# Kernel optimization log

Measured on AMD Instinct MI355X. Metric: run time of the kernel, lower is better.

Reference implementation:

```python
import jax, jax.numpy as jnp
import numpy as np

N_SRC = 50000
N_DST = 50000
E = 640000
D_IN = 128
D_OUT = 128
H = 4
D_HEAD = D_OUT // H


def setup_inputs() -> dict:
    key = jax.random.key(0)
    k1, k2, k3, k4, k5, k6 = jax.random.split(key, 6)
    src_feat = jax.random.normal(k1, (N_SRC, D_IN), dtype=jnp.float32)
    dst_feat = jax.random.normal(k2, (N_DST, D_IN), dtype=jnp.float32)
    src_idx = jax.random.randint(k3, (E,), 0, N_SRC)
    dst_idx = jax.random.randint(k4, (E,), 0, N_DST)
    edge_index = jnp.stack([src_idx, dst_idx], axis=0)  # [2, E]
    # nn.Linear(d_in, d_out, bias=False): store as [d_in, d_out] so h = x @ W
    W = jax.random.normal(k5, (D_IN, D_OUT), dtype=jnp.float32) * (1.0 / np.sqrt(D_IN))
    # nn.Linear(2*d_head, 1, bias=False): attention vector of length 2*d_head
    a = jax.random.normal(k6, (2 * D_HEAD,), dtype=jnp.float32) * (1.0 / np.sqrt(2 * D_HEAD))
    return {"src_feat": src_feat, "dst_feat": dst_feat, "edge_index": edge_index,
            "W": W, "a": a, "num_dst": N_DST}


def reference(src_feat, dst_feat, edge_index, W, a, num_dst):
    # Dropout in eval mode (identity).
    d_out = W.shape[1]
    d_head = d_out // H
    src_idx = edge_index[0]
    dst_idx = edge_index[1]

    h_src = (src_feat @ W).reshape(-1, H, d_head)  # [N_src, H, d_head]
    h_dst = (dst_feat @ W).reshape(-1, H, d_head)  # [N_dst, H, d_head]
    h_src_e = h_src[src_idx]                        # [E, H, d_head]
    h_dst_e = h_dst[dst_idx]                        # [E, H, d_head]

    # a^T [h_src || h_dst] == h_src . a_src + h_dst . a_dst (shared across heads)
    a_src, a_dst = a[:d_head], a[d_head:]
    e = jax.nn.elu(jnp.einsum('ehd,d->eh', h_src_e, a_src)
                   + jnp.einsum('ehd,d->eh', h_dst_e, a_dst))  # [E, H]

    # Segment softmax over edges grouped by destination node.
    e_max = jax.ops.segment_max(e, dst_idx, num_segments=num_dst)      # [N_dst, H]
    exp_e = jnp.exp(e - e_max[dst_idx])
    denom = jax.ops.segment_sum(exp_e, dst_idx, num_segments=num_dst)  # [N_dst, H]
    alpha = exp_e / (denom[dst_idx] + 1e-12)                           # [E, H]

    # Scatter-add of weighted messages.
    out = jax.ops.segment_sum(alpha[..., None] * h_src_e, dst_idx,
                              num_segments=num_dst)                    # [N_dst, H, d_head]
    return out.reshape(num_dst, d_out)
```

## Files before the change

### kernel.cpp

```cpp
#include <hip/hip_runtime.h>
#include <math.h>

constexpr int N_SRC_ = 50000;
constexpr int N_DST_ = 50000;
constexpr int N_TOT_ = 100000;
constexpr int E_     = 640000;
constexpr int D_     = 128;
constexpr int CAP_   = 64;
constexpr int NTILE  = (N_SRC_ + 31) / 32;
constexpr int MMB    = (NTILE + 3) / 4;

typedef float f32x4  __attribute__((ext_vector_type(4)));
typedef short bf16x8 __attribute__((ext_vector_type(8)));

union U4 { unsigned int u[4]; bf16x8 v; };

static __device__ __forceinline__ unsigned short f2bf_rne(float f) {
    unsigned int x = __float_as_uint(f);
    return (unsigned short)((x + 0x7FFFu + ((x >> 16) & 1u)) >> 16);
}

__global__ __launch_bounds__(256) void k_s2v(
    const float* __restrict__ src, const float* __restrict__ dst,
    const float* __restrict__ W, const float* __restrict__ a,
    float* __restrict__ s, int* __restrict__ cursor)
{
    __shared__ float val[128 * 8];
    const int t = threadIdx.x;

    int cid = blockIdx.x * 256 + t;
    if (cid < N_DST_) cursor[cid] = 0;

#pragma unroll
    for (int j = 0; j < 4; ++j) {
        int pair = t * 4 + j;
        int k = pair >> 3, col = pair & 7;
        int half = col >> 2, hd = col & 3;
        float acc = 0.f;
        for (int c2 = 0; c2 < 32; ++c2)
            acc += W[(size_t)k * 128 + hd * 32 + c2] * a[half * 32 + c2];
        val[k * 8 + col] = acc;
    }
    __syncthreads();

    const int gw = (blockIdx.x * 256 + t) >> 6;
    const int lane = t & 63;
    const int l32 = lane & 31, hf = lane >> 5;

    float4 vs[4], vd[4];
#pragma unroll
    for (int j = 0; j < 4; ++j) {
        vs[j] = *(const float4*)&val[(4 * l32 + j) * 8];
        vd[j] = *(const float4*)&val[(4 * l32 + j) * 8 + 4];
    }

    for (int p = gw; p < N_TOT_ / 2; p += 2048) {
        int node = p * 2 + hf;
        bool is_src = node < N_SRC_;
        const float* f = is_src ? src + (size_t)node * D_
                                : dst + (size_t)(node - N_SRC_) * D_;
        float4 x = *(const float4*)(f + l32 * 4);
        float4 v0 = is_src ? vs[0] : vd[0];
        float4 v1 = is_src ? vs[1] : vd[1];
        float4 v2 = is_src ? vs[2] : vd[2];
        float4 v3 = is_src ? vs[3] : vd[3];
        float a0 = x.x * v0.x + x.y * v1.x + x.z * v2.x + x.w * v3.x;
        float a1 = x.x * v0.y + x.y * v1.y + x.z * v2.y + x.w * v3.y;
        float a2 = x.x * v0.z + x.y * v1.z + x.z * v2.z + x.w * v3.z;
        float a3 = x.x * v0.w + x.y * v1.w + x.z * v2.w + x.w * v3.w;
#pragma unroll
        for (int m = 1; m < 32; m <<= 1) {
            a0 += __shfl_xor(a0, m, 64);
            a1 += __shfl_xor(a1, m, 64);
            a2 += __shfl_xor(a2, m, 64);
            a3 += __shfl_xor(a3, m, 64);
        }
        if (l32 == 0)
            *(float4*)&s[(size_t)node * 4] = make_float4(a0, a1, a2, a3);
    }
}

__global__ __launch_bounds__(256) void k_mm(
    const float* __restrict__ src, const float* __restrict__ W,
    unsigned int* __restrict__ h)
{
    __shared__ unsigned short wl[128 * 128];
    const int t = threadIdx.x;
    {
        const int n = t >> 1, half = t & 1;
#pragma unroll
        for (int c8 = 0; c8 < 8; ++c8) {
            int c = half * 8 + c8;
            U4 P;
#pragma unroll
            for (int q = 0; q < 4; ++q) {
                float f0 = W[(size_t)(c * 8 + 2 * q) * 128 + n];
                float f1 = W[(size_t)(c * 8 + 2 * q + 1) * 128 + n];
                P.u[q] = (unsigned int)f2bf_rne(f0)
                       | ((unsigned int)f2bf_rne(f1) << 16);
            }
            int slot = c ^ (n & 15);
            *(bf16x8*)&wl[n * 128 + slot * 8] = P.v;
        }
    }
    __syncthreads();

    const int wid = t >> 6, lane = t & 63;
    const int g = lane >> 4, sidx = lane & 15;
    const int wtile = blockIdx.x * 4 + wid;
    if (wtile >= NTILE) return;
    const int base = wtile * 32;
    const int r0 = base + sidx;
    const int r1g = base + 16 + sidx;
    const int r1 = (r1g < N_SRC_) ? r1g : 0;
    const float* p0 = src + (size_t)r0 * D_;
    const float* p1 = src + (size_t)r1 * D_;

    f32x4 acc[2][8];
#pragma unroll
    for (int m = 0; m < 2; ++m)
#pragma unroll
        for (int nf = 0; nf < 8; ++nf) acc[m][nf] = (f32x4)0.f;

#pragma unroll
    for (int ks = 0; ks < 4; ++ks) {
        const int k0 = ks * 32 + g * 8;
        bf16x8 af[2];
#pragma unroll
        for (int m = 0; m < 2; ++m) {
            const float* p = m ? p1 : p0;
            float4 v0 = *(const float4*)(p + k0);
            float4 v1 = *(const float4*)(p + k0 + 4);
            float f[8] = {v0.x, v0.y, v0.z, v0.w, v1.x, v1.y, v1.z, v1.w};
            U4 P;
#pragma unroll
            for (int q = 0; q < 4; ++q)
                P.u[q] = (unsigned int)f2bf_rne(f[2 * q])
                       | ((unsigned int)f2bf_rne(f[2 * q + 1]) << 16);
            af[m] = P.v;
        }
#pragma unroll
        for (int nf = 0; nf < 8; ++nf) {
            const int n = nf * 16 + sidx;
            const int off = n * 128 + ((ks * 4 + g) ^ sidx) * 8;
            bf16x8 b = *(const bf16x8*)&wl[off];
            acc[0][nf] = __builtin_amdgcn_mfma_f32_16x16x32_bf16(af[0], b, acc[0][nf], 0, 0, 0);
            acc[1][nf] = __builtin_amdgcn_mfma_f32_16x16x32_bf16(af[1], b, acc[1][nf], 0, 0, 0);
        }
    }

#pragma unroll
    for (int m = 0; m < 2; ++m) {
        const int rowb = base + m * 16 + g * 4;
#pragma unroll
        for (int r = 0; r < 4; ++r) {
            const int row = rowb + r;
            if (row < N_SRC_) {
#pragma unroll
                for (int q = 0; q < 4; ++q) {
                    unsigned int val = (unsigned int)f2bf_rne(acc[m][2 * q][r])
                                     | ((unsigned int)f2bf_rne(acc[m][2 * q + 1][r]) << 16);
                    h[(size_t)row * 64 + q * 16 + sidx] = val;
                }
            }
        }
    }
}

__global__ __launch_bounds__(256) void k_scatter(
    const int* __restrict__ src_idx, const int* __restrict__ dst_idx,
    const float* __restrict__ s,
    int* __restrict__ cursor, uint4* __restrict__ bucket)
{
    int e = blockIdx.x * 256 + threadIdx.x;
    int sn = src_idx[e], dn = dst_idx[e];
    float4 vsv = *(const float4*)&s[(size_t)sn * 4];
    float4 vdv = *(const float4*)&s[(size_t)(N_SRC_ + dn) * 4];
    float x0 = vsv.x + vdv.x, x1 = vsv.y + vdv.y;
    float x2 = vsv.z + vdv.z, x3 = vsv.w + vdv.w;
    float w0 = __expf(x0 > 0.f ? x0 : (__expf(x0) - 1.f));
    float w1 = __expf(x1 > 0.f ? x1 : (__expf(x1) - 1.f));
    float w2 = __expf(x2 > 0.f ? x2 : (__expf(x2) - 1.f));
    float w3 = __expf(x3 > 0.f ? x3 : (__expf(x3) - 1.f));
    uint4 ent;
    ent.x = (unsigned int)sn;
    ent.y = (unsigned int)f2bf_rne(w0) | ((unsigned int)f2bf_rne(w1) << 16);
    ent.z = (unsigned int)f2bf_rne(w2) | ((unsigned int)f2bf_rne(w3) << 16);
    ent.w = 0u;
    int pos = atomicAdd(&cursor[dn], 1);
    if (pos < CAP_) bucket[(size_t)dn * CAP_ + pos] = ent;
}

__global__ __launch_bounds__(256) void k_gather(
    const unsigned int* __restrict__ h2, const int* __restrict__ cursor,
    const uint4* __restrict__ bucket, float* __restrict__ out)
{
    int wid = (blockIdx.x * 256 + threadIdx.x) >> 6;
    int lane = threadIdx.x & 63;
    if (wid >= N_DST_) return;
    int cnt = min(cursor[wid], CAP_);
    const int hd = lane >> 4;
    const int sub = lane & 15;
    const uint4* B = bucket + (size_t)wid * CAP_;

    auto wext = [&](const uint4& e) {
        unsigned int u = (hd & 2) ? e.z : e.y;
        return __uint_as_float((hd & 1) ? (u & 0xFFFF0000u) : (u << 16));
    };

    float2 A[4] = {make_float2(0.f, 0.f), make_float2(0.f, 0.f),
                   make_float2(0.f, 0.f), make_float2(0.f, 0.f)};
    float dacc[4] = {0.f, 0.f, 0.f, 0.f};

    int i = 0;
    for (; i + 8 <= cnt; i += 8) {
        uint4 e[8];
        unsigned int v[8];
#pragma unroll
        for (int j = 0; j < 8; ++j) e[j] = B[i + j];
#pragma unroll
        for (int j = 0; j < 8; ++j) v[j] = h2[(size_t)e[j].x * 64 + lane];
#pragma unroll
        for (int j = 0; j < 8; ++j) {
            float w = wext(e[j]);
            dacc[j & 3] += w;
            A[j & 3].x = fmaf(w, __uint_as_float(v[j] << 16), A[j & 3].x);
            A[j & 3].y = fmaf(w, __uint_as_float(v[j] & 0xFFFF0000u), A[j & 3].y);
        }
    }
    for (; i + 4 <= cnt; i += 4) {
        uint4 e[4];
        unsigned int v[4];
#pragma unroll
        for (int j = 0; j < 4; ++j) e[j] = B[i + j];
#pragma unroll
        for (int j = 0; j < 4; ++j) v[j] = h2[(size_t)e[j].x * 64 + lane];
#pragma unroll
        for (int j = 0; j < 4; ++j) {
            float w = wext(e[j]);
            dacc[j] += w;
            A[j].x = fmaf(w, __uint_as_float(v[j] << 16), A[j].x);
            A[j].y = fmaf(w, __uint_as_float(v[j] & 0xFFFF0000u), A[j].y);
        }
    }
    for (; i < cnt; ++i) {
        uint4 e = B[i];
        unsigned int v = h2[(size_t)e.x * 64 + lane];
        float w = wext(e);
        dacc[0] += w;
        A[0].x = fmaf(w, __uint_as_float(v << 16), A[0].x);
        A[0].y = fmaf(w, __uint_as_float(v & 0xFFFF0000u), A[0].y);
    }

    float den = (dacc[0] + dacc[1]) + (dacc[2] + dacc[3]);
    float2 acc = make_float2((A[0].x + A[1].x) + (A[2].x + A[3].x),
                             (A[0].y + A[1].y) + (A[2].y + A[3].y));
    float inv = 1.f / (den + 1e-12f);
    out[(size_t)wid * D_ + 32 * hd + sub]      = acc.x * inv;
    out[(size_t)wid * D_ + 32 * hd + sub + 16] = acc.y * inv;
}

extern "C" void kernel_launch(void* const* d_in, const int* in_sizes, int n_in,
                              void* d_out, int out_size, void* d_ws, size_t ws_size,
                              hipStream_t stream)
{
    const float* src_feat = (const float*)d_in[0];
    const float* dst_feat = (const float*)d_in[1];
    const int*   edge     = (const int*)d_in[2];
    const int*   src_idx  = edge;
    const int*   dst_idx  = edge + E_;
    const float* W        = (const float*)d_in[3];
    const float* a        = (const float*)d_in[4];
    float*       out      = (float*)d_out;

    char* p = (char*)d_ws;
    auto alloc = [&](size_t bytes) {
        char* r = p;
        p += (bytes + 255) & ~(size_t)255;
        return r;
    };
    unsigned int* h = (unsigned int*)alloc((size_t)N_SRC_ * 64 * 4);
    float* s        = (float*)alloc((size_t)N_TOT_ * 4 * sizeof(float));
    int*   cursor   = (int*)alloc((size_t)N_DST_ * sizeof(int));
    uint4* bucket   = (uint4*)alloc((size_t)N_DST_ * CAP_ * sizeof(uint4));

    k_s2v<<<512, 256, 0, stream>>>(src_feat, dst_feat, W, a, s, cursor);
    k_mm<<<MMB, 256, 0, stream>>>(src_feat, W, h);
    k_scatter<<<E_ / 256, 256, 0, stream>>>(src_idx, dst_idx, s, cursor, bucket);
    k_gather<<<(N_DST_ * 64 + 255) / 256, 256, 0, stream>>>(
        h, cursor, bucket, out);
}
```

Before: 215.3 us.

## Fuse four GAT kernels into one cooperative persistent kernel with grid syncs

Replaces the four launches (score/cursor init, bf16 MFMA projection, edge scatter into buckets, per-destination gather) with a single cooperative kernel. The grid is sized from an occupancy query and split in half so the score pass and the matmul pass run concurrently, with grid-wide barriers before the scatter and gather phases. This removes launch gaps and overlaps the two independent front stages. In exchange it adds grid.sync overhead and persistent-loop scheduling, and keeps the old multi-kernel path as a fallback if the cooperative launch fails.

New measurement: 408.8 us. +89.9%, slower.

```diff
diff --git a/kernel.cpp b/kernel.cpp
--- a/kernel.cpp
+++ b/kernel.cpp
@@ -1,5 +1,8 @@
 #include <hip/hip_runtime.h>
+#include <hip/hip_cooperative_groups.h>
 #include <math.h>
+
+namespace cg = cooperative_groups;
 
 constexpr int N_SRC_ = 50000;
 constexpr int N_DST_ = 50000;
@@ -20,6 +23,237 @@
     return (unsigned short)((x + 0x7FFFu + ((x >> 16) & 1u)) >> 16);
 }
 
+__global__ __launch_bounds__(256, 4) void k_fused(
+    const float* __restrict__ src, const float* __restrict__ dstf,
+    const int* __restrict__ src_idx, const int* __restrict__ dst_idx,
+    const float* __restrict__ W, const float* __restrict__ a,
+    float* __restrict__ s, int* __restrict__ cursor,
+    uint4* __restrict__ bucket, unsigned int* __restrict__ h,
+    float* __restrict__ out)
+{
+    cg::grid_group grid = cg::this_grid();
+    __shared__ unsigned short wl[128 * 128];
+    const int t  = threadIdx.x;
+    const int NB = (int)gridDim.x;
+    const int SB = NB >> 1;
+
+    if ((int)blockIdx.x < SB) {
+        float* val = (float*)wl;
+        for (int cid = blockIdx.x * 256 + t; cid < N_DST_; cid += SB * 256)
+            cursor[cid] = 0;
+#pragma unroll
+        for (int j = 0; j < 4; ++j) {
+            int pair = t * 4 + j;
+            int k = pair >> 3, col = pair & 7;
+            int half = col >> 2, hd = col & 3;
+            float acc = 0.f;
+            for (int c2 = 0; c2 < 32; ++c2)
+                acc += W[(size_t)k * 128 + hd * 32 + c2] * a[half * 32 + c2];
+            val[k * 8 + col] = acc;
+        }
+        __syncthreads();
+
+        const int lane = t & 63;
+        const int l32 = lane & 31, hf = lane >> 5;
+        float4 vs[4], vd[4];
+#pragma unroll
+        for (int j = 0; j < 4; ++j) {
+            vs[j] = *(const float4*)&val[(4 * l32 + j) * 8];
+            vd[j] = *(const float4*)&val[(4 * l32 + j) * 8 + 4];
+        }
+        const int gw = (blockIdx.x * 256 + t) >> 6;
+        const int stride = SB * 4;
+        for (int p = gw; p < N_TOT_ / 2; p += stride) {
+            int node = p * 2 + hf;
+            bool is_src = node < N_SRC_;
+            const float* f = is_src ? src + (size_t)node * D_
+                                    : dstf + (size_t)(node - N_SRC_) * D_;
+            float4 x = *(const float4*)(f + l32 * 4);
+            float4 v0 = is_src ? vs[0] : vd[0];
+            float4 v1 = is_src ? vs[1] : vd[1];
+            float4 v2 = is_src ? vs[2] : vd[2];
+            float4 v3 = is_src ? vs[3] : vd[3];
+            float a0 = x.x * v0.x + x.y * v1.x + x.z * v2.x + x.w * v3.x;
+            float a1 = x.x * v0.y + x.y * v1.y + x.z * v2.y + x.w * v3.y;
+            float a2 = x.x * v0.z + x.y * v1.z + x.z * v2.z + x.w * v3.z;
+            float a3 = x.x * v0.w + x.y * v1.w + x.z * v2.w + x.w * v3.w;
+#pragma unroll
+            for (int m = 1; m < 32; m <<= 1) {
+                a0 += __shfl_xor(a0, m, 64);
+                a1 += __shfl_xor(a1, m, 64);
+                a2 += __shfl_xor(a2, m, 64);
+                a3 += __shfl_xor(a3, m, 64);
+            }
+            if (l32 == 0)
+                *(float4*)&s[(size_t)node * 4] = make_float4(a0, a1, a2, a3);
+        }
+    } else {
+        {
+            const int n = t >> 1, half = t & 1;
+#pragma unroll
+            for (int c8 = 0; c8 < 8; ++c8) {
+                int c = half * 8 + c8;
+                U4 P;
+#pragma unroll
+                for (int q = 0; q < 4; ++q) {
+                    float f0 = W[(size_t)(c * 8 + 2 * q) * 128 + n];
+                    float f1 = W[(size_t)(c * 8 + 2 * q + 1) * 128 + n];
+                    P.u[q] = (unsigned int)f2bf_rne(f0)
+                           | ((unsigned int)f2bf_rne(f1) << 16);
+                }
+                int slot = c ^ (n & 15);
+                *(bf16x8*)&wl[n * 128 + slot * 8] = P.v;
+            }
+        }
+        __syncthreads();
+
+        const int wid = t >> 6, lane = t & 63;
+        const int g = lane >> 4, sidx = lane & 15;
+        for (int wtile = ((int)blockIdx.x - SB) * 4 + wid; wtile < NTILE;
+             wtile += (NB - SB) * 4) {
+            const int base = wtile * 32;
+            const int r0 = base + sidx;
+            const int r1g = base + 16 + sidx;
+            const int r1 = (r1g < N_SRC_) ? r1g : 0;
+            const float* p0 = src + (size_t)r0 * D_;
+            const float* p1 = src + (size_t)r1 * D_;
+
+            f32x4 acc[2][8];
+#pragma unroll
+            for (int m = 0; m < 2; ++m)
+#pragma unroll
+                for (int nf = 0; nf < 8; ++nf) acc[m][nf] = (f32x4)0.f;
+
+#pragma unroll
+            for (int ks = 0; ks < 4; ++ks) {
+                const int k0 = ks * 32 + g * 8;
+                bf16x8 af[2];
+#pragma unroll
+                for (int m = 0; m < 2; ++m) {
+                    const float* p = m ? p1 : p0;
+                    float4 v0 = *(const float4*)(p + k0);
+                    float4 v1 = *(const float4*)(p + k0 + 4);
+                    float f[8] = {v0.x, v0.y, v0.z, v0.w, v1.x, v1.y, v1.z, v1.w};
+                    U4 P;
+#pragma unroll
+                    for (int q = 0; q < 4; ++q)
+                        P.u[q] = (unsigned int)f2bf_rne(f[2 * q])
+                               | ((unsigned int)f2bf_rne(f[2 * q + 1]) << 16);
+                    af[m] = P.v;
+                }
+#pragma unroll
+                for (int nf = 0; nf < 8; ++nf) {
+                    const int n = nf * 16 + sidx;
+                    const int off = n * 128 + ((ks * 4 + g) ^ sidx) * 8;
+                    bf16x8 b = *(const bf16x8*)&wl[off];
+                    acc[0][nf] = __builtin_amdgcn_mfma_f32_16x16x32_bf16(af[0], b, acc[0][nf], 0, 0, 0);
+                    acc[1][nf] = __builtin_amdgcn_mfma_f32_16x16x32_bf16(af[1], b, acc[1][nf], 0, 0, 0);
+                }
+            }
+#pragma unroll
+            for (int m = 0; m < 2; ++m) {
+                const int rowb = base + m * 16 + g * 4;
+#pragma unroll
+                for (int r = 0; r < 4; ++r) {
+                    const int row = rowb + r;
+                    if (row < N_SRC_) {
+#pragma unroll
+                        for (int q = 0; q < 4; ++q) {
+                            unsigned int val2 = (unsigned int)f2bf_rne(acc[m][2 * q][r])
+                                             | ((unsigned int)f2bf_rne(acc[m][2 * q + 1][r]) << 16);
+                            h[(size_t)row * 64 + q * 16 + sidx] = val2;
+                        }
+                    }
+                }
+            }
+        }
+    }
+
+    grid.sync();
+
+    for (int e = blockIdx.x * 256 + t; e < E_; e += NB * 256) {
+        int sn = src_idx[e], dn = dst_idx[e];
+        float4 vsv = *(const float4*)&s[(size_t)sn * 4];
+        float4 vdv = *(const float4*)&s[(size_t)(N_SRC_ + dn) * 4];
+        float x0 = vsv.x + vdv.x, x1 = vsv.y + vdv.y;
+        float x2 = vsv.z + vdv.z, x3 = vsv.w + vdv.w;
+        float w0 = __expf(x0 > 0.f ? x0 : (__expf(x0) - 1.f));
+        float w1 = __expf(x1 > 0.f ? x1 : (__expf(x1) - 1.f));
+        float w2 = __expf(x2 > 0.f ? x2 : (__expf(x2) - 1.f));
+        float w3 = __expf(x3 > 0.f ? x3 : (__expf(x3) - 1.f));
+        uint4 ent;
+        ent.x = (unsigned int)sn;
+        ent.y = (unsigned int)f2bf_rne(w0) | ((unsigned int)f2bf_rne(w1) << 16);
+        ent.z = (unsigned int)f2bf_rne(w2) | ((unsigned int)f2bf_rne(w3) << 16);
+        ent.w = 0u;
+        int pos = atomicAdd(&cursor[dn], 1);
+        if (pos < CAP_) bucket[(size_t)dn * CAP_ + pos] = ent;
+    }
+
+    grid.sync();
+
+    {
+        const int lane = t & 63;
+        const int hd = lane >> 4, sub = lane & 15;
+        for (int wid = (blockIdx.x * 256 + t) >> 6; wid < N_DST_; wid += NB * 4) {
+            int cnt = min(cursor[wid], CAP_);
+            const uint4* B = bucket + (size_t)wid * CAP_;
+            auto wext = [&](const uint4& e) {
+                unsigned int u = (hd & 2) ? e.z : e.y;
+                return __uint_as_float((hd & 1) ? (u & 0xFFFF0000u) : (u << 16));
+            };
+            float2 A[4] = {make_float2(0.f, 0.f), make_float2(0.f, 0.f),
+                           make_float2(0.f, 0.f), make_float2(0.f, 0.f)};
+            float dacc[4] = {0.f, 0.f, 0.f, 0.f};
+            int i = 0;
+            for (; i + 8 <= cnt; i += 8) {
+                uint4 e[8];
+                unsigned int v[8];
+#pragma unroll
+                for (int j = 0; j < 8; ++j) e[j] = B[i + j];
+#pragma unroll
+                for (int j = 0; j < 8; ++j) v[j] = h[(size_t)e[j].x * 64 + lane];
+#pragma unroll
+                for (int j = 0; j < 8; ++j) {
+                    float w = wext(e[j]);
+                    dacc[j & 3] += w;
+                    A[j & 3].x = fmaf(w, __uint_as_float(v[j] << 16), A[j & 3].x);
+                    A[j & 3].y = fmaf(w, __uint_as_float(v[j] & 0xFFFF0000u), A[j & 3].y);
+                }
+            }
+            for (; i + 4 <= cnt; i += 4) {
+                uint4 e[4];
+                unsigned int v[4];
+#pragma unroll
+                for (int j = 0; j < 4; ++j) e[j] = B[i + j];
+#pragma unroll
+                for (int j = 0; j < 4; ++j) v[j] = h[(size_t)e[j].x * 64 + lane];
+#pragma unroll
+                for (int j = 0; j < 4; ++j) {
+                    float w = wext(e[j]);
+                    dacc[j] += w;
+                    A[j].x = fmaf(w, __uint_as_float(v[j] << 16), A[j].x);
+                    A[j].y = fmaf(w, __uint_as_float(v[j] & 0xFFFF0000u), A[j].y);
+                }
+            }
+            for (; i < cnt; ++i) {
+                uint4 e = B[i];
+                unsigned int v = h[(size_t)e.x * 64 + lane];
+                float w = wext(e);
+                dacc[0] += w;
+                A[0].x = fmaf(w, __uint_as_float(v << 16), A[0].x);
+                A[0].y = fmaf(w, __uint_as_float(v & 0xFFFF0000u), A[0].y);
+            }
+            float den = (dacc[0] + dacc[1]) + (dacc[2] + dacc[3]);
+            float2 acc = make_float2((A[0].x + A[1].x) + (A[2].x + A[3].x),
+                                     (A[0].y + A[1].y) + (A[2].y + A[3].y));
+            float inv = 1.f / (den + 1e-12f);
+            out[(size_t)wid * D_ + 32 * hd + sub]      = acc.x * inv;
+            out[(size_t)wid * D_ + 32 * hd + sub + 16] = acc.y * inv;
+        }
+    }
+}
+
 __global__ __launch_bounds__(256) void k_s2v(
     const float* __restrict__ src, const float* __restrict__ dst,
     const float* __restrict__ W, const float* __restrict__ a,
@@ -27,10 +261,8 @@
 {
     __shared__ float val[128 * 8];
     const int t = threadIdx.x;
-
     int cid = blockIdx.x * 256 + t;
     if (cid < N_DST_) cursor[cid] = 0;
-
 #pragma unroll
     for (int j = 0; j < 4; ++j) {
         int pair = t * 4 + j;
@@ -42,18 +274,15 @@
         val[k * 8 + col] = acc;
     }
     __syncthreads();
-
     const int gw = (blockIdx.x * 256 + t) >> 6;
     const int lane = t & 63;
     const int l32 = lane & 31, hf = lane >> 5;
-
     float4 vs[4], vd[4];
 #pragma unroll
     for (int j = 0; j < 4; ++j) {
         vs[j] = *(const float4*)&val[(4 * l32 + j) * 8];
         vd[j] = *(const float4*)&val[(4 * l32 + j) * 8 + 4];
     }
-
     for (int p = gw; p < N_TOT_ / 2; p += 2048) {
         int node = p * 2 + hf;
         bool is_src = node < N_SRC_;
@@ -104,7 +333,6 @@
         }
     }
     __syncthreads();
-
     const int wid = t >> 6, lane = t & 63;
     const int g = lane >> 4, sidx = lane & 15;
     const int wtile = blockIdx.x * 4 + wid;
@@ -115,13 +343,11 @@
     const int r1 = (r1g < N_SRC_) ? r1g : 0;
     const float* p0 = src + (size_t)r0 * D_;
     const float* p1 = src + (size_t)r1 * D_;
-
     f32x4 acc[2][8];
 #pragma unroll
     for (int m = 0; m < 2; ++m)
 #pragma unroll
         for (int nf = 0; nf < 8; ++nf) acc[m][nf] = (f32x4)0.f;
-
 #pragma unroll
     for (int ks = 0; ks < 4; ++ks) {
         const int k0 = ks * 32 + g * 8;
@@ -148,7 +374,6 @@
             acc[1][nf] = __builtin_amdgcn_mfma_f32_16x16x32_bf16(af[1], b, acc[1][nf], 0, 0, 0);
         }
     }
-
 #pragma unroll
     for (int m = 0; m < 2; ++m) {
         const int rowb = base + m * 16 + g * 4;
@@ -202,16 +427,13 @@
     const int hd = lane >> 4;
     const int sub = lane & 15;
     const uint4* B = bucket + (size_t)wid * CAP_;
-
     auto wext = [&](const uint4& e) {
         unsigned int u = (hd & 2) ? e.z : e.y;
         return __uint_as_float((hd & 1) ? (u & 0xFFFF0000u) : (u << 16));
     };
-
     float2 A[4] = {make_float2(0.f, 0.f), make_float2(0.f, 0.f),
                    make_float2(0.f, 0.f), make_float2(0.f, 0.f)};
     float dacc[4] = {0.f, 0.f, 0.f, 0.f};
-
     int i = 0;
     for (; i + 8 <= cnt; i += 8) {
         uint4 e[8];
@@ -251,7 +473,6 @@
         A[0].x = fmaf(w, __uint_as_float(v << 16), A[0].x);
         A[0].y = fmaf(w, __uint_as_float(v & 0xFFFF0000u), A[0].y);
     }
-
     float den = (dacc[0] + dacc[1]) + (dacc[2] + dacc[3]);
     float2 acc = make_float2((A[0].x + A[1].x) + (A[2].x + A[3].x),
                              (A[0].y + A[1].y) + (A[2].y + A[3].y));
@@ -284,9 +505,25 @@
     int*   cursor   = (int*)alloc((size_t)N_DST_ * sizeof(int));
     uint4* bucket   = (uint4*)alloc((size_t)N_DST_ * CAP_ * sizeof(uint4));
 
-    k_s2v<<<512, 256, 0, stream>>>(src_feat, dst_feat, W, a, s, cursor);
-    k_mm<<<MMB, 256, 0, stream>>>(src_feat, W, h);
-    k_scatter<<<E_ / 256, 256, 0, stream>>>(src_idx, dst_idx, s, cursor, bucket);
-    k_gather<<<(N_DST_ * 64 + 255) / 256, 256, 0, stream>>>(
-        h, cursor, bucket, out);
-}
+    int perCU = 0;
+    hipError_t qerr = hipOccupancyMaxActiveBlocksPerMultiprocessor(
+        &perCU, (const void*)k_fused, 256, 0);
+    int NB = (qerr == hipSuccess && perCU > 0) ? perCU * 256 : 1024;
+    if (NB > 1024) NB = 1024;
+    NB &= ~1;
+    if (NB < 2) NB = 2;
+
+    void* args[] = {(void*)&src_feat, (void*)&dst_feat, (void*)&src_idx,
+                    (void*)&dst_idx, (void*)&W, (void*)&a, (void*)&s,
+                    (void*)&cursor, (void*)&bucket, (void*)&h, (void*)&out};
+    hipError_t err = hipLaunchCooperativeKernel(
+        (const void*)k_fused, dim3(NB), dim3(256), args, 0, stream);
+
+    if (err != hipSuccess) {
+        k_s2v<<<512, 256, 0, stream>>>(src_feat, dst_feat, W, a, s, cursor);
+        k_mm<<<MMB, 256, 0, stream>>>(src_feat, W, h);
+        k_scatter<<<E_ / 256, 256, 0, stream>>>(src_idx, dst_idx, s, cursor, bucket);
+        k_gather<<<(N_DST_ * 64 + 255) / 256, 256, 0, stream>>>(
+            h, cursor, bucket, out);
+    }
+}
```
